# Kernel optimization log

Measured on AMD Instinct MI355X. Metric: run time of the kernel, lower is better.

The kernel has to match this reference:

```python
import jax, jax.numpy as jnp
import numpy as np

B, N_TOK, D = 32, 1024, 1024
CH, PS, NP = 3, 16, 32  # channels, patch_size, n_patches (sample_size // patch_size)
EPS = 1e-5


def setup_inputs() -> dict:
    key = jax.random.key(0)
    k1, k2 = jax.random.split(key)
    x = jax.random.normal(k1, (B, N_TOK, D), dtype=jnp.float32)
    ln_w = jnp.ones((D,), dtype=jnp.float32)
    ln_b = jnp.zeros((D,), dtype=jnp.float32)
    W = jax.random.normal(k2, (CH * PS * PS, D), dtype=jnp.float32) * (1.0 / np.sqrt(D))
    b = jnp.zeros((CH * PS * PS,), dtype=jnp.float32)
    return {"x": x, "ln_w": ln_w, "ln_b": ln_b, "W": W, "b": b}


def reference(x, ln_w, ln_b, W, b):
    # LayerNorm over last dim
    mean = jnp.mean(x, axis=-1, keepdims=True)
    var = jnp.mean(jnp.square(x - mean), axis=-1, keepdims=True)
    h = (x - mean) * jax.lax.rsqrt(var + EPS) * ln_w + ln_b
    # SiLU
    h = h * jax.nn.sigmoid(h)
    # Linear: [B, N, D] @ [D, ph*pw*c] + bias
    y = jnp.einsum('bnd,od->bno', h, W) + b  # [B, N_TOK, PS*PS*CH]
    # rearrange 'b (h w) (ph pw c) -> b c (h ph) (w pw)'
    y = y.reshape(B, NP, NP, PS, PS, CH)           # b h w ph pw c
    y = y.transpose(0, 5, 1, 3, 2, 4)              # b c h ph w pw
    y = y.reshape(B, CH, NP * PS, NP * PS)
    return y
```

## Files before the change

### kernel.cpp

```cpp
#include <hip/hip_runtime.h>
#include <hip/hip_bf16.h>

#define M_TOT 32768
#define DDIM  1024
#define ODIM  768
#define LN_EPS 1e-5f

typedef __attribute__((__ext_vector_type__(8))) short bf16x8;
typedef __attribute__((__ext_vector_type__(4))) float f32x4;

__device__ __forceinline__ unsigned short f2bf(float f) {
  union { __hip_bfloat16 h; unsigned short u; } cv;
  cv.h = __float2bfloat16(f);
  return cv.u;
}

__device__ __forceinline__ float silu_f(float v) {
  return v / (1.f + __expf(-v));
}

__global__ __launch_bounds__(256)
void ln_silu_kernel(const float* __restrict__ x, const float* __restrict__ lnw,
                    const float* __restrict__ lnb, __hip_bfloat16* __restrict__ h,
                    const float4* __restrict__ Wf, ushort4* __restrict__ Wb)
{
  const int tid  = threadIdx.x;

  if (blockIdx.x >= 8192) {
    const int i = (blockIdx.x - 8192) * 256 + tid;
    float4 v = Wf[i];
    ushort4 o;
    o.x = f2bf(v.x); o.y = f2bf(v.y); o.z = f2bf(v.z); o.w = f2bf(v.w);
    Wb[i] = o;
    return;
  }

  const int lane = tid & 63;
  const int wid  = tid >> 6;
  const int row  = blockIdx.x * 4 + wid;

  const float4* xr = (const float4*)(x + (size_t)row * DDIM);
  float4 v[4];
#pragma unroll
  for (int jj = 0; jj < 4; ++jj) v[jj] = xr[lane + 64 * jj];

  float s = 0.f, ss = 0.f;
#pragma unroll
  for (int jj = 0; jj < 4; ++jj) {
    float4 a = v[jj];
    s  += a.x + a.y + a.z + a.w;
    ss += a.x * a.x + a.y * a.y + a.z * a.z + a.w * a.w;
  }
#pragma unroll
  for (int off = 1; off < 64; off <<= 1) {
    s  += __shfl_xor(s, off);
    ss += __shfl_xor(ss, off);
  }
  const float mean = s * (1.f / 1024.f);
  const float rstd = rsqrtf(ss * (1.f / 1024.f) - mean * mean + LN_EPS);

  ushort4* hr = (ushort4*)(h + (size_t)row * DDIM);
#pragma unroll
  for (int jj = 0; jj < 4; ++jj) {
    float4 wv = ((const float4*)lnw)[lane + 64 * jj];
    float4 bv = ((const float4*)lnb)[lane + 64 * jj];
    float4 a  = v[jj];
    float e0 = silu_f((a.x - mean) * rstd * wv.x + bv.x);
    float e1 = silu_f((a.y - mean) * rstd * wv.y + bv.y);
    float e2 = silu_f((a.z - mean) * rstd * wv.z + bv.z);
    float e3 = silu_f((a.w - mean) * rstd * wv.w + bv.w);
    ushort4 o; o.x = f2bf(e0); o.y = f2bf(e1); o.z = f2bf(e2); o.w = f2bf(e3);
    hr[lane + 64 * jj] = o;
  }
}

#define GBM 128
#define GBN 192
#define GBK 64
#define ABY  16384
#define BUFB 40960

__device__ __forceinline__ void gload16(const void* g, void* l) {
  __builtin_amdgcn_global_load_lds(
      (const __attribute__((address_space(1))) unsigned int*)g,
      (__attribute__((address_space(3))) unsigned int*)l, 16, 0, 0);
}

#define VMW(n) asm volatile("s_waitcnt vmcnt(" #n ")" ::: "memory")

__global__ __launch_bounds__(256, 2)
void gemm_kernel(const __hip_bfloat16* __restrict__ h,
                 const __hip_bfloat16* __restrict__ Wb,
                 const float* __restrict__ bias,
                 float* __restrict__ out)
{
  __shared__ char smem[2 * BUFB];
  const int tid  = threadIdx.x;
  const int lane = tid & 63;
  const int w    = tid >> 6;

  const int wg = blockIdx.x;
  const int sv = ((wg & 7) << 7) + (wg >> 3);
  const int mt = sv >> 2, nt = sv & 3;
  const int m0 = mt << 7, n0 = nt * GBN;

  const __hip_bfloat16* aP[4]; int aD[4];
#pragma unroll
  for (int q = 0; q < 4; ++q) {
    int s = (q << 8) + tid;
    int row = s >> 3, chk = s & 7;
    aP[q] = h + (size_t)(m0 + row) * DDIM + ((chk ^ (row & 7)) << 3);
    aD[q] = s << 4;
  }
  const __hip_bfloat16* bP[6]; int bD[6];
#pragma unroll
  for (int q = 0; q < 6; ++q) {
    int s = (q << 8) + tid;
    int row = s >> 3, chk = s & 7;
    bP[q] = Wb + (size_t)(n0 + row) * DDIM + ((chk ^ (row & 7)) << 3);
    bD[q] = ABY + (s << 4);
  }

  const int wm = w >> 1, wn = w & 1;
  const int lr = lane & 15, lq = lane >> 4;
  int aRd[8], bRd[12];
#pragma unroll
  for (int kk = 0; kk < 2; ++kk) {
#pragma unroll
    for (int i = 0; i < 4; ++i) {
      int row = wm * 64 + i * 16 + lr;
      aRd[kk * 4 + i] = row * 128 + ((((kk << 2) | lq) ^ (row & 7)) << 4);
    }
#pragma unroll
    for (int j = 0; j < 6; ++j) {
      int row = wn * 96 + j * 16 + lr;
      bRd[kk * 6 + j] = ABY + row * 128 + ((((kk << 2) | lq) ^ (row & 7)) << 4);
    }
  }

  auto stage = [&](int t) {
    char* b = smem + (t & 1) * BUFB;
    const int k0 = t << 6;
#pragma unroll
    for (int q = 0; q < 4; ++q) gload16(aP[q] + k0, b + aD[q]);
#pragma unroll
    for (int q = 0; q < 6; ++q) gload16(bP[q] + k0, b + bD[q]);
  };

  f32x4 acc[4][6];
#pragma unroll
  for (int i = 0; i < 4; ++i)
#pragma unroll
    for (int j = 0; j < 6; ++j)
      acc[i][j] = (f32x4){0.f, 0.f, 0.f, 0.f};

  stage(0);

  for (int t = 0; t < 16; ++t) {
    VMW(0);
    __builtin_amdgcn_s_barrier();
    asm volatile("" ::: "memory");

    const char* bb = smem + (t & 1) * BUFB;
    if (t < 15) stage(t + 1);
    bf16x8 af[4], bfq[6];
#pragma unroll
    for (int i = 0; i < 4; ++i) af[i]  = *(const bf16x8*)(bb + aRd[i]);
#pragma unroll
    for (int j = 0; j < 6; ++j) bfq[j] = *(const bf16x8*)(bb + bRd[j]);
    __builtin_amdgcn_s_setprio(1);
#pragma unroll
    for (int i = 0; i < 4; ++i)
#pragma unroll
      for (int j = 0; j < 6; ++j)
        acc[i][j] = __builtin_amdgcn_mfma_f32_16x16x32_bf16(af[i], bfq[j], acc[i][j], 0, 0, 0);
    __builtin_amdgcn_s_setprio(0);
#pragma unroll
    for (int i = 0; i < 4; ++i) af[i]  = *(const bf16x8*)(bb + aRd[4 + i]);
#pragma unroll
    for (int j = 0; j < 6; ++j) bfq[j] = *(const bf16x8*)(bb + bRd[6 + j]);
    __builtin_amdgcn_s_setprio(1);
#pragma unroll
    for (int i = 0; i < 4; ++i)
#pragma unroll
      for (int j = 0; j < 6; ++j)
        acc[i][j] = __builtin_amdgcn_mfma_f32_16x16x32_bf16(af[i], bfq[j], acc[i][j], 0, 0, 0);
    __builtin_amdgcn_s_setprio(0);
  }

  const int b   = m0 >> 10;
  const int hl0 = (m0 & 1023) >> 5;
  float bv[6]; int cj[6], pwj[6], prj[6];
#pragma unroll
  for (int j = 0; j < 6; ++j) {
    int o = wn * 96 + j * 16 + lr;
    bv[j]  = bias[n0 + o];
    cj[j]  = o % 3;
    int oq = o / 3;
    pwj[j] = oq & 15;
    prj[j] = oq >> 4;
  }

#pragma unroll
  for (int gp = 0; gp < 4; ++gp) {
    {
      float* dst = (float*)(smem + (wm << 14));
#pragma unroll
      for (int j = 0; j < 6; ++j)
#pragma unroll
        for (int r = 0; r < 4; ++r) {
          const int tk = lq * 4 + r;
          dst[((cj[j] * 4 + prj[j]) << 8) + (tk << 4) + (pwj[j] ^ (lq << 2))] =
              acc[gp][j][r] + bv[j];
        }
    }
    __syncthreads();
#pragma unroll
    for (int half = 0; half < 2; ++half) {
      const int g  = (half << 2) + gp;
      const int hh = hl0 + (g >> 1);
      const float* src = (const float*)(smem + (half << 14));
#pragma unroll
      for (int u = 0; u < 3; ++u) {
        const int f   = (u << 8) + tid;
        const int c   = u;
        const int pr  = (f >> 6) & 3;
        const int tk  = (f >> 2) & 15;
        const int pw0 = (f & 3) << 2;
        const int lqw = tk >> 2;
        float4 v = *(const float4*)(src + (((c * 4 + pr) << 8) + (tk << 4)
                                           + (pw0 ^ (lqw << 2))));
        const size_t idx = (((size_t)(b * 3 + c)) << 18)
                         + (size_t)((hh << 4) + (nt << 2) + pr) * 512
                         + ((g & 1) << 8) + (tk << 4) + pw0;
        *(float4*)(out + idx) = v;
      }
    }
    __syncthreads();
  }
}

#define BM 64
#define BK 32
#define NTHR 1024
#define LDS_BYTES 53760

__global__ __launch_bounds__(NTHR, 4)
void fused_kernel(const float* __restrict__ x,
                  const float* __restrict__ lnw,
                  const float* __restrict__ lnb,
                  const float* __restrict__ Wf,
                  const float* __restrict__ bias,
                  float* __restrict__ out)
{
  extern __shared__ char smem[];
  char* AsBase = smem;
  char* BsBase = smem + 4096;
  float* smean = (float*)(smem + 53248);
  float* srstd = smean + BM;

  const int tid = threadIdx.x;
  const int m0  = blockIdx.x * BM;
  const int bb   = m0 >> 10;
  const int h0   = (m0 & 1023) >> 5;

  {
    const int row = tid >> 4;
    const int sub = tid & 15;
    const float4* xr = (const float4*)(x + (size_t)(m0 + row) * DDIM);
    float s = 0.f, ss = 0.f;
#pragma unroll 4
    for (int j = 0; j < 16; ++j) {
      float4 v = xr[sub + (j << 4)];
      s  += v.x + v.y + v.z + v.w;
      ss += v.x * v.x + v.y * v.y + v.z * v.z + v.w * v.w;
    }
#pragma unroll
    for (int off = 1; off < 16; off <<= 1) {
      s  += __shfl_xor(s, off);
      ss += __shfl_xor(ss, off);
    }
    if (sub == 0) {
      float mean = s * (1.f / 1024.f);
      float var  = ss * (1.f / 1024.f) - mean * mean;
      smean[row] = mean;
      srstd[row] = rsqrtf(var + LN_EPS);
    }
  }
  __syncthreads();

  const int arow  = tid >> 4;
  const int acol2 = tid & 15;
  const int aOff  = (m0 + arow) * DDIM + (acol2 << 1);
  const int aDst  = (arow << 6) + ((((acol2 >> 2) ^ ((arow >> 2) & 3)) << 4)) + ((acol2 & 3) << 2);
  const float aMean = smean[arow];
  const float aRstd = srstd[arow];

  int bOffF[6], bDstF[6];
#pragma unroll
  for (int c = 0; c < 6; ++c) {
    int idx = tid + (c << 10);
    int r = idx >> 3, c4 = idx & 7;
    bOffF[c] = r * DDIM + (c4 << 2);
    bDstF[c] = (r << 6) + ((((c4 >> 1) ^ ((r >> 2) & 3)) << 4)) + ((c4 & 1) << 3);
  }

  const int lane = tid & 63;
  const int wid  = tid >> 6;
  const int lr   = lane & 15;
  const int lq   = lane >> 4;
  const int kswz = (lq ^ ((lr >> 2) & 3)) << 4;
  int aRd[4], bRd[3];
#pragma unroll
  for (int i = 0; i < 4; ++i) aRd[i] = (((i << 4) + lr) << 6) + kswz;
#pragma unroll
  for (int j = 0; j < 3; ++j) bRd[j] = ((wid * 48 + (j << 4) + lr) << 6) + kswz;

  float2 aReg, lwReg, lbReg;
  float4 bRegF[6];

  auto loadTile = [&](int tt) {
    const int k0 = tt * BK;
    aReg  = *(const float2*)(x + aOff + k0);
    lwReg = *(const float2*)(lnw + (acol2 << 1) + k0);
    lbReg = *(const float2*)(lnb + (acol2 << 1) + k0);
#pragma unroll
    for (int c = 0; c < 6; ++c)
      bRegF[c] = *(const float4*)(Wf + bOffF[c] + k0);
  };

  auto storeTile = [&]() {
    float hx = (aReg.x - aMean) * aRstd * lwReg.x + lbReg.x;
    float hy = (aReg.y - aMean) * aRstd * lwReg.y + lbReg.y;
    hx = silu_f(hx); hy = silu_f(hy);
    ushort2 ap; ap.x = f2bf(hx); ap.y = f2bf(hy);
    *(ushort2*)(AsBase + aDst) = ap;
#pragma unroll
    for (int c = 0; c < 6; ++c) {
      float4 wv = bRegF[c];
      ushort4 bp; bp.x = f2bf(wv.x); bp.y = f2bf(wv.y); bp.z = f2bf(wv.z); bp.w = f2bf(wv.w);
      *(ushort4*)(BsBase + bDstF[c]) = bp;
    }
  };

  f32x4 acc[4][3];
#pragma unroll
  for (int i = 0; i < 4; ++i)
#pragma unroll
    for (int j = 0; j < 3; ++j)
      acc[i][j] = (f32x4){0.f, 0.f, 0.f, 0.f};

  loadTile(0);
  storeTile();
  __syncthreads();

  for (int t = 0; t < 32; ++t) {
    if (t < 31) loadTile(t + 1);
    bf16x8 af[4], bfr[3];
#pragma unroll
    for (int i = 0; i < 4; ++i) af[i] = *(const bf16x8*)(AsBase + aRd[i]);
#pragma unroll
    for (int j = 0; j < 3; ++j) bfr[j] = *(const bf16x8*)(BsBase + bRd[j]);
#pragma unroll
    for (int i = 0; i < 4; ++i)
#pragma unroll
      for (int j = 0; j < 3; ++j)
        acc[i][j] = __builtin_amdgcn_mfma_f32_16x16x32_bf16(af[i], bfr[j], acc[i][j], 0, 0, 0);
    __syncthreads();
    if (t < 31) storeTile();
    __syncthreads();
  }

  float* ldsF = (float*)smem;
  float bv[3]; int cv[3], phv[3], pwv[3];
#pragma unroll
  for (int j = 0; j < 3; ++j) {
    const int o = wid * 48 + (j << 4) + lr;
    bv[j]  = bias[o];
    cv[j]  = o % 3;
    const int oq = o / 3;
    pwv[j] = oq & 15;
    phv[j] = oq >> 4;
  }

#pragma unroll
  for (int i = 0; i < 4; ++i) {
#pragma unroll
    for (int j = 0; j < 3; ++j) {
#pragma unroll
      for (int r = 0; r < 4; ++r) {
        const int wl  = (lq << 2) + r;
        const int lin = ((cv[j] * 16 + phv[j]) << 8) + (wl << 4) + pwv[j];
        const int dws = lin ^ (cv[j] << 2) ^ (((lin >> 6) & 1) << 4);
        ldsF[dws] = acc[i][j][r] + bv[j];
      }
    }
    __syncthreads();
    const int hq = h0 + (i >> 1);
    const int w0 = (i & 1) << 4;
#pragma unroll
    for (int q = 0; q < 3; ++q) {
      const int g4  = (q << 10) + tid;
      const int dw  = g4 << 2;
      const int run = dw >> 8;
      const int c   = run >> 4;
      const int ph  = run & 15;
      const int wl  = (dw >> 4) & 15;
      const int pw  = dw & 15;
      const int dws = dw ^ (c << 2) ^ (((dw >> 6) & 1) << 4);
      float4 v = *(const float4*)(ldsF + dws);
      const size_t idx = (((size_t)(bb * 3 + c)) << 18)
                       + ((size_t)((hq << 4) + ph) << 9)
                       + ((w0 + wl) << 4) + pw;
      *(float4*)(out + idx) = v;
    }
    __syncthreads();
  }
}

extern "C" void kernel_launch(void* const* d_in, const int* in_sizes, int n_in,
                              void* d_out, int out_size, void* d_ws, size_t ws_size,
                              hipStream_t stream) {
  const float* x    = (const float*)d_in[0];
  const float* lnw  = (const float*)d_in[1];
  const float* lnb  = (const float*)d_in[2];
  const float* W    = (const float*)d_in[3];
  const float* bias = (const float*)d_in[4];
  float* out = (float*)d_out;

  const size_t wbBytes = (size_t)ODIM * DDIM * sizeof(__hip_bfloat16);
  const size_t hBytes  = (size_t)M_TOT * DDIM * sizeof(__hip_bfloat16);
  __hip_bfloat16* Wb = (__hip_bfloat16*)d_ws;
  __hip_bfloat16* hb = (__hip_bfloat16*)((char*)d_ws + wbBytes);

  if (ws_size >= wbBytes + hBytes) {
    ln_silu_kernel<<<dim3(8192 + 768), dim3(256), 0, stream>>>(
        x, lnw, lnb, hb, (const float4*)W, (ushort4*)Wb);
    gemm_kernel<<<dim3((M_TOT / GBM) * (ODIM / GBN)), dim3(256), 0, stream>>>(hb, Wb, bias, out);
  } else {
    fused_kernel<<<dim3(M_TOT / BM), dim3(NTHR), LDS_BYTES, stream>>>(
        x, lnw, lnb, W, bias, out);
  }
}
```

Before: 98.20 us.

## Fuse LayerNorm+SiLU into GEMM producer warps, dropping bf16 activation buffer

The bf16 activation tensor is no longer written to memory. A lighter first kernel computes only per-row mean and rstd, converts W to bf16, and packs the LN weight and bias. The GEMM gains two producer warps that read fp32 x, apply LayerNorm and SiLU, and write bf16 A tiles into swizzled LDS, while the compute warps stage only W. This removes the activation write and re-read, but each x row is re-read and re-normalized by every one of the four N-tile blocks. It also raises the block to 384 threads.

```diff
diff --git a/kernel.cpp b/kernel.cpp
--- a/kernel.cpp
+++ b/kernel.cpp
@@ -15,39 +15,53 @@
   return cv.u;
 }
 
+__device__ __forceinline__ int pk2(float a, float b) {
+  return (int)((unsigned)f2bf(a) | ((unsigned)f2bf(b) << 16));
+}
+
+__device__ __forceinline__ float bflo(unsigned u) {
+  union { float f; unsigned v; } c; c.v = u << 16; return c.f;
+}
+__device__ __forceinline__ float bfhi(unsigned u) {
+  union { float f; unsigned v; } c; c.v = u & 0xFFFF0000u; return c.f;
+}
+
 __device__ __forceinline__ float silu_f(float v) {
   return v / (1.f + __expf(-v));
 }
 
 __global__ __launch_bounds__(256)
-void ln_silu_kernel(const float* __restrict__ x, const float* __restrict__ lnw,
-                    const float* __restrict__ lnb, __hip_bfloat16* __restrict__ h,
-                    const float4* __restrict__ Wf, ushort4* __restrict__ Wb)
+void stats_kernel(const float* __restrict__ x, const float* __restrict__ lnw,
+                  const float* __restrict__ lnb, float* __restrict__ sm,
+                  float* __restrict__ sr, unsigned* __restrict__ wbpk,
+                  const float4* __restrict__ Wf, ushort4* __restrict__ Wb)
 {
-  const int tid  = threadIdx.x;
-
-  if (blockIdx.x >= 8192) {
-    const int i = (blockIdx.x - 8192) * 256 + tid;
-    float4 v = Wf[i];
-    ushort4 o;
-    o.x = f2bf(v.x); o.y = f2bf(v.y); o.z = f2bf(v.z); o.w = f2bf(v.w);
-    Wb[i] = o;
+  const int tid = threadIdx.x;
+  const int bid = blockIdx.x;
+  if (bid >= 8192) {
+    if (bid < 8960) {
+      const int i = ((bid - 8192) << 8) + tid;
+      float4 v = Wf[i];
+      ushort4 o;
+      o.x = f2bf(v.x); o.y = f2bf(v.y); o.z = f2bf(v.z); o.w = f2bf(v.w);
+      Wb[i] = o;
+    } else {
+#pragma unroll
+      for (int q = 0; q < 4; ++q) {
+        const int k = (q << 8) + tid;
+        wbpk[k] = (unsigned)f2bf(lnw[k]) | ((unsigned)f2bf(lnb[k]) << 16);
+      }
+    }
     return;
   }
-
   const int lane = tid & 63;
   const int wid  = tid >> 6;
-  const int row  = blockIdx.x * 4 + wid;
-
+  const int row  = (bid << 2) + wid;
   const float4* xr = (const float4*)(x + (size_t)row * DDIM);
-  float4 v[4];
-#pragma unroll
-  for (int jj = 0; jj < 4; ++jj) v[jj] = xr[lane + 64 * jj];
-
   float s = 0.f, ss = 0.f;
 #pragma unroll
   for (int jj = 0; jj < 4; ++jj) {
-    float4 a = v[jj];
+    float4 a = xr[lane + 64 * jj];
     s  += a.x + a.y + a.z + a.w;
     ss += a.x * a.x + a.y * a.y + a.z * a.z + a.w * a.w;
   }
@@ -56,21 +70,10 @@
     s  += __shfl_xor(s, off);
     ss += __shfl_xor(ss, off);
   }
-  const float mean = s * (1.f / 1024.f);
-  const float rstd = rsqrtf(ss * (1.f / 1024.f) - mean * mean + LN_EPS);
-
-  ushort4* hr = (ushort4*)(h + (size_t)row * DDIM);
-#pragma unroll
-  for (int jj = 0; jj < 4; ++jj) {
-    float4 wv = ((const float4*)lnw)[lane + 64 * jj];
-    float4 bv = ((const float4*)lnb)[lane + 64 * jj];
-    float4 a  = v[jj];
-    float e0 = silu_f((a.x - mean) * rstd * wv.x + bv.x);
-    float e1 = silu_f((a.y - mean) * rstd * wv.y + bv.y);
-    float e2 = silu_f((a.z - mean) * rstd * wv.z + bv.z);
-    float e3 = silu_f((a.w - mean) * rstd * wv.w + bv.w);
-    ushort4 o; o.x = f2bf(e0); o.y = f2bf(e1); o.z = f2bf(e2); o.w = f2bf(e3);
-    hr[lane + 64 * jj] = o;
+  if (lane == 0) {
+    const float mean = s * (1.f / 1024.f);
+    sm[row] = mean;
+    sr[row] = rsqrtf(ss * (1.f / 1024.f) - mean * mean + LN_EPS);
   }
 }
 
@@ -88,8 +91,10 @@
 
 #define VMW(n) asm volatile("s_waitcnt vmcnt(" #n ")" ::: "memory")
 
-__global__ __launch_bounds__(256, 2)
-void gemm_kernel(const __hip_bfloat16* __restrict__ h,
+__global__ __launch_bounds__(384, 3)
+void gemm_kernel(const float* __restrict__ x,
+                 const float* __restrict__ sm, const float* __restrict__ sr,
+                 const unsigned* __restrict__ wbpk,
                  const __hip_bfloat16* __restrict__ Wb,
                  const float* __restrict__ bias,
                  float* __restrict__ out)
@@ -104,48 +109,8 @@
   const int mt = sv >> 2, nt = sv & 3;
   const int m0 = mt << 7, n0 = nt * GBN;
 
-  const __hip_bfloat16* aP[4]; int aD[4];
-#pragma unroll
-  for (int q = 0; q < 4; ++q) {
-    int s = (q << 8) + tid;
-    int row = s >> 3, chk = s & 7;
-    aP[q] = h + (size_t)(m0 + row) * DDIM + ((chk ^ (row & 7)) << 3);
-    aD[q] = s << 4;
-  }
-  const __hip_bfloat16* bP[6]; int bD[6];
-#pragma unroll
-  for (int q = 0; q < 6; ++q) {
-    int s = (q << 8) + tid;
-    int row = s >> 3, chk = s & 7;
-    bP[q] = Wb + (size_t)(n0 + row) * DDIM + ((chk ^ (row & 7)) << 3);
-    bD[q] = ABY + (s << 4);
-  }
-
   const int wm = w >> 1, wn = w & 1;
   const int lr = lane & 15, lq = lane >> 4;
-  int aRd[8], bRd[12];
-#pragma unroll
-  for (int kk = 0; kk < 2; ++kk) {
-#pragma unroll
-    for (int i = 0; i < 4; ++i) {
-      int row = wm * 64 + i * 16 + lr;
-      aRd[kk * 4 + i] = row * 128 + ((((kk << 2) | lq) ^ (row & 7)) << 4);
-    }
-#pragma unroll
-    for (int j = 0; j < 6; ++j) {
-      int row = wn * 96 + j * 16 + lr;
-      bRd[kk * 6 + j] = ABY + row * 128 + ((((kk << 2) | lq) ^ (row & 7)) << 4);
-    }
-  }
-
-  auto stage = [&](int t) {
-    char* b = smem + (t & 1) * BUFB;
-    const int k0 = t << 6;
-#pragma unroll
-    for (int q = 0; q < 4; ++q) gload16(aP[q] + k0, b + aD[q]);
-#pragma unroll
-    for (int q = 0; q < 6; ++q) gload16(bP[q] + k0, b + bD[q]);
-  };
 
   f32x4 acc[4][6];
 #pragma unroll
@@ -154,38 +119,122 @@
     for (int j = 0; j < 6; ++j)
       acc[i][j] = (f32x4){0.f, 0.f, 0.f, 0.f};
 
-  stage(0);
-
-  for (int t = 0; t < 16; ++t) {
+  if (w >= 4) {
+    const int p  = tid & 127;
+    const int rB = p >> 4;
+    const int k4 = p & 15;
+    float mu[16], rs[16];
+#pragma unroll
+    for (int i = 0; i < 16; ++i) {
+      const int r = rB + (i << 3);
+      mu[i] = sm[m0 + r];
+      rs[i] = sr[m0 + r];
+    }
+    const float* xb = x + (size_t)(m0 + rB) * DDIM + (k4 << 2);
+    float4 xv[16];
+    uint4  wbr;
+    auto ploadx = [&](int kt) {
+#pragma unroll
+      for (int i = 0; i < 16; ++i)
+        xv[i] = *(const float4*)(xb + (size_t)(i << 3) * DDIM + (kt << 6));
+      wbr = *(const uint4*)(wbpk + (kt << 6) + (k4 << 2));
+    };
+    auto pwrite = [&](int kt) {
+      char* dstb = smem + (kt & 1) * BUFB;
+      const int kc = k4 >> 1, hv = k4 & 1;
+      const float w0 = bflo(wbr.x), b0 = bfhi(wbr.x);
+      const float w1 = bflo(wbr.y), b1 = bfhi(wbr.y);
+      const float w2 = bflo(wbr.z), b2 = bfhi(wbr.z);
+      const float w3 = bflo(wbr.w), b3 = bfhi(wbr.w);
+#pragma unroll
+      for (int i = 0; i < 16; ++i) {
+        const int r = rB + (i << 3);
+        float4 xx = xv[i];
+        const float h0 = silu_f((xx.x - mu[i]) * rs[i] * w0 + b0);
+        const float h1 = silu_f((xx.y - mu[i]) * rs[i] * w1 + b1);
+        const float h2 = silu_f((xx.z - mu[i]) * rs[i] * w2 + b2);
+        const float h3 = silu_f((xx.w - mu[i]) * rs[i] * w3 + b3);
+        int2 pk; pk.x = pk2(h0, h1); pk.y = pk2(h2, h3);
+        *(int2*)(dstb + r * 128 + ((kc ^ (r & 7)) << 4) + (hv << 3)) = pk;
+      }
+    };
+    ploadx(0);
     VMW(0);
-    __builtin_amdgcn_s_barrier();
-    asm volatile("" ::: "memory");
-
-    const char* bb = smem + (t & 1) * BUFB;
-    if (t < 15) stage(t + 1);
-    bf16x8 af[4], bfq[6];
-#pragma unroll
-    for (int i = 0; i < 4; ++i) af[i]  = *(const bf16x8*)(bb + aRd[i]);
-#pragma unroll
-    for (int j = 0; j < 6; ++j) bfq[j] = *(const bf16x8*)(bb + bRd[j]);
-    __builtin_amdgcn_s_setprio(1);
-#pragma unroll
-    for (int i = 0; i < 4; ++i)
-#pragma unroll
-      for (int j = 0; j < 6; ++j)
-        acc[i][j] = __builtin_amdgcn_mfma_f32_16x16x32_bf16(af[i], bfq[j], acc[i][j], 0, 0, 0);
-    __builtin_amdgcn_s_setprio(0);
-#pragma unroll
-    for (int i = 0; i < 4; ++i) af[i]  = *(const bf16x8*)(bb + aRd[4 + i]);
-#pragma unroll
-    for (int j = 0; j < 6; ++j) bfq[j] = *(const bf16x8*)(bb + bRd[6 + j]);
-    __builtin_amdgcn_s_setprio(1);
-#pragma unroll
-    for (int i = 0; i < 4; ++i)
-#pragma unroll
-      for (int j = 0; j < 6; ++j)
-        acc[i][j] = __builtin_amdgcn_mfma_f32_16x16x32_bf16(af[i], bfq[j], acc[i][j], 0, 0, 0);
-    __builtin_amdgcn_s_setprio(0);
+    pwrite(0);
+    ploadx(1);
+    asm volatile("s_waitcnt lgkmcnt(0)" ::: "memory");
+    for (int t = 0; t < 16; ++t) {
+      __builtin_amdgcn_s_barrier();
+      asm volatile("" ::: "memory");
+      if (t < 15) {
+        VMW(0);
+        pwrite(t + 1);
+        if (t < 14) ploadx(t + 2);
+        asm volatile("s_waitcnt lgkmcnt(0)" ::: "memory");
+      }
+    }
+  } else {
+    const __hip_bfloat16* bP[6]; int bD[6];
+#pragma unroll
+    for (int q = 0; q < 6; ++q) {
+      int s = (q << 8) + tid;
+      int row = s >> 3, chk = s & 7;
+      bP[q] = Wb + (size_t)(n0 + row) * DDIM + ((chk ^ (row & 7)) << 3);
+      bD[q] = ABY + (s << 4);
+    }
+    int aRd[8], bRd[12];
+#pragma unroll
+    for (int kk = 0; kk < 2; ++kk) {
+#pragma unroll
+      for (int i = 0; i < 4; ++i) {
+        int row = wm * 64 + i * 16 + lr;
+        aRd[kk * 4 + i] = row * 128 + ((((kk << 2) | lq) ^ (row & 7)) << 4);
+      }
+#pragma unroll
+      for (int j = 0; j < 6; ++j) {
+        int row = wn * 96 + j * 16 + lr;
+        bRd[kk * 6 + j] = ABY + row * 128 + ((((kk << 2) | lq) ^ (row & 7)) << 4);
+      }
+    }
+    auto stageB = [&](int t) {
+      char* b = smem + (t & 1) * BUFB;
+      const int k0 = t << 6;
+#pragma unroll
+      for (int q = 0; q < 6; ++q) gload16(bP[q] + k0, b + bD[q]);
+    };
+
+    stageB(0);
+    for (int t = 0; t < 16; ++t) {
+      VMW(0);
+      __builtin_amdgcn_s_barrier();
+      asm volatile("" ::: "memory");
+
+      const char* bb = smem + (t & 1) * BUFB;
+      if (t < 15) stageB(t + 1);
+      bf16x8 af[4], bfq[6];
+#pragma unroll
+      for (int i = 0; i < 4; ++i) af[i]  = *(const bf16x8*)(bb + aRd[i]);
+#pragma unroll
+      for (int j = 0; j < 6; ++j) bfq[j] = *(const bf16x8*)(bb + bRd[j]);
+      __builtin_amdgcn_s_setprio(1);
+#pragma unroll
+      for (int i = 0; i < 4; ++i)
+#pragma unroll
+        for (int j = 0; j < 6; ++j)
+          acc[i][j] = __builtin_amdgcn_mfma_f32_16x16x32_bf16(af[i], bfq[j], acc[i][j], 0, 0, 0);
+      __builtin_amdgcn_s_setprio(0);
+#pragma unroll
+      for (int i = 0; i < 4; ++i) af[i]  = *(const bf16x8*)(bb + aRd[4 + i]);
+#pragma unroll
+      for (int j = 0; j < 6; ++j) bfq[j] = *(const bf16x8*)(bb + bRd[6 + j]);
+      __builtin_amdgcn_s_setprio(1);
+#pragma unroll
+      for (int i = 0; i < 4; ++i)
+#pragma unroll
+        for (int j = 0; j < 6; ++j)
+          acc[i][j] = __builtin_amdgcn_mfma_f32_16x16x32_bf16(af[i], bfq[j], acc[i][j], 0, 0, 0);
+      __builtin_amdgcn_s_setprio(0);
+    }
   }
 
   const int b   = m0 >> 10;
@@ -203,8 +252,8 @@
 
 #pragma unroll
   for (int gp = 0; gp < 4; ++gp) {
-    {
-      float* dst = (float*)(smem + (wm << 14));
+    if (w < 4 && wm == 0) {
+      float* dst = (float*)(smem);
 #pragma unroll
       for (int j = 0; j < 6; ++j)
 #pragma unroll
@@ -214,26 +263,39 @@
               acc[gp][j][r] + bv[j];
         }
     }
+    if (w < 4 && wm == 1) {
+      float* dst = (float*)(smem + 16384);
+#pragma unroll
+      for (int j = 0; j < 6; ++j)
+#pragma unroll
+        for (int r = 0; r < 4; ++r) {
+          const int tk = lq * 4 + r;
+          dst[((cj[j] * 4 + prj[j]) << 8) + (tk << 4) + (pwj[j] ^ (lq << 2))] =
+              acc[gp][j][r] + bv[j];
+        }
+    }
     __syncthreads();
-#pragma unroll
-    for (int half = 0; half < 2; ++half) {
-      const int g  = (half << 2) + gp;
-      const int hh = hl0 + (g >> 1);
-      const float* src = (const float*)(smem + (half << 14));
-#pragma unroll
-      for (int u = 0; u < 3; ++u) {
-        const int f   = (u << 8) + tid;
-        const int c   = u;
-        const int pr  = (f >> 6) & 3;
-        const int tk  = (f >> 2) & 15;
-        const int pw0 = (f & 3) << 2;
-        const int lqw = tk >> 2;
-        float4 v = *(const float4*)(src + (((c * 4 + pr) << 8) + (tk << 4)
-                                           + (pw0 ^ (lqw << 2))));
-        const size_t idx = (((size_t)(b * 3 + c)) << 18)
-                         + (size_t)((hh << 4) + (nt << 2) + pr) * 512
-                         + ((g & 1) << 8) + (tk << 4) + pw0;
-        *(float4*)(out + idx) = v;
+    if (tid < 256) {
+#pragma unroll
+      for (int half2 = 0; half2 < 2; ++half2) {
+        const int g  = (half2 << 2) + gp;
+        const int hh = hl0 + (g >> 1);
+        const float* src = (const float*)(smem + (half2 << 14));
+#pragma unroll
+        for (int u = 0; u < 3; ++u) {
+          const int f   = (u << 8) + tid;
+          const int c   = u;
+          const int pr  = (f >> 6) & 3;
+          const int tk  = (f >> 2) & 15;
+          const int pw0 = (f & 3) << 2;
+          const int lqw = tk >> 2;
+          float4 v = *(const float4*)(src + (((c * 4 + pr) << 8) + (tk << 4)
+                                             + (pw0 ^ (lqw << 2))));
+          const size_t idx = (((size_t)(b * 3 + c)) << 18)
+                           + (size_t)((hh << 4) + (nt << 2) + pr) * 512
+                           + ((g & 1) << 8) + (tk << 4) + pw0;
+          *(float4*)(out + idx) = v;
+        }
       }
     }
     __syncthreads();
@@ -429,14 +491,17 @@
   float* out = (float*)d_out;
 
   const size_t wbBytes = (size_t)ODIM * DDIM * sizeof(__hip_bfloat16);
-  const size_t hBytes  = (size_t)M_TOT * DDIM * sizeof(__hip_bfloat16);
-  __hip_bfloat16* Wb = (__hip_bfloat16*)d_ws;
-  __hip_bfloat16* hb = (__hip_bfloat16*)((char*)d_ws + wbBytes);
-
-  if (ws_size >= wbBytes + hBytes) {
-    ln_silu_kernel<<<dim3(8192 + 768), dim3(256), 0, stream>>>(
-        x, lnw, lnb, hb, (const float4*)W, (ushort4*)Wb);
-    gemm_kernel<<<dim3((M_TOT / GBM) * (ODIM / GBN)), dim3(256), 0, stream>>>(hb, Wb, bias, out);
+  const size_t stBytes = (size_t)M_TOT * sizeof(float);
+  __hip_bfloat16* Wb  = (__hip_bfloat16*)d_ws;
+  float* sm           = (float*)((char*)d_ws + wbBytes);
+  float* sr           = (float*)((char*)d_ws + wbBytes + stBytes);
+  unsigned* wbpk      = (unsigned*)((char*)d_ws + wbBytes + 2 * stBytes);
+
+  if (ws_size >= wbBytes + 2 * stBytes + DDIM * sizeof(unsigned)) {
+    stats_kernel<<<dim3(8192 + 768 + 1), dim3(256), 0, stream>>>(
+        x, lnw, lnb, sm, sr, wbpk, (const float4*)W, (ushort4*)Wb);
+    gemm_kernel<<<dim3((M_TOT / GBM) * (ODIM / GBN)), dim3(384), 0, stream>>>(
+        x, sm, sr, wbpk, Wb, bias, out);
   } else {
     fused_kernel<<<dim3(M_TOT / BM), dim3(NTHR), LDS_BYTES, stream>>>(
         x, lnw, lnb, W, bias, out);
```

New measurement: 238.6 us. 143% more time.
